# Kernel optimization log

Hardware: AMD Instinct MI355X
Metric: run time of the kernel (lower is better)

## Reference

```python
import jax, jax.numpy as jnp
import numpy as np

NEG_INF = -1e9  # matches tf mask value -1000000000.0
LEAKY_ALPHA = 0.2  # tf.nn.leaky_relu default


def setup_inputs() -> dict:
    key = jax.random.key(0)
    k1, k2, k3, k4 = jax.random.split(key, 4)
    B, N, F, U = 8, 2048, 128, 128
    X = jax.random.normal(k1, (B, N, F), dtype=jnp.float32)
    A = jax.random.randint(k2, (B, N, N), 0, 2, dtype=jnp.int32)
    W = jax.random.normal(k3, (F, U), dtype=jnp.float32) * 0.1
    a = jax.random.normal(k4, (2 * U, 1), dtype=jnp.float32) * 0.1
    return {"X": X, "A": A, "W": W, "a": a}


def reference(X, A, W, a):
    # H = X @ W : [B, N, U]
    H = jnp.einsum('bnf,fu->bnu', X, W)
    U = H.shape[-1]
    # Additive decomposition of the tile+concat: [H_i || H_j] @ a = H_i@a_src + H_j@a_dst
    a_src = a[:U, 0]   # [U]
    a_dst = a[U:, 0]   # [U]
    s = H @ a_src      # [B, N]
    t = H @ a_dst      # [B, N]
    e = s[:, :, None] + t[:, None, :]            # [B, N, N] pairwise logits
    e = jax.nn.leaky_relu(e, negative_slope=LEAKY_ALPHA)
    mask = jnp.where(A > 0, 0.0, NEG_INF).astype(e.dtype)
    attention = jax.nn.softmax(e + mask, axis=-1)  # [B, N, N]
    H_out = jnp.einsum('bij,bju->biu', attention, H)
    return jax.nn.relu(H_out)
```

## Files before the change

kernel.cpp:

```cpp
#include <hip/hip_runtime.h>
#include <hip/hip_bf16.h>


#define NEG_INF -1.0e9f

typedef __bf16 bf16x8 __attribute__((ext_vector_type(8)));
typedef unsigned short ushort8 __attribute__((ext_vector_type(8)));
typedef float f32x4 __attribute__((ext_vector_type(4)));

__device__ __forceinline__ unsigned short f2b(float x) {
    unsigned u = __builtin_bit_cast(unsigned, x);
    u += 0x7fffu + ((u >> 16) & 1u);
    return (unsigned short)(u >> 16);
}

__device__ __forceinline__ void gload_lds16(const void* g, void* l) {
    __builtin_amdgcn_global_load_lds(
        (const __attribute__((address_space(1))) void*)g,
        (__attribute__((address_space(3))) void*)l, 16, 0, 0);
}

__global__ __launch_bounds__(256) void k_h(const float* __restrict__ X,
                                           const float* __restrict__ W,
                                           const float* __restrict__ a,
                                           unsigned short* __restrict__ HT,
                                           float* __restrict__ sbuf,
                                           float* __restrict__ tbuf) {
    __shared__ unsigned short WT[128 * 136];

    const int tid  = threadIdx.x;
    const int w    = tid >> 6;
    const int lane = tid & 63;
    const int r    = lane & 15;
    const int cg   = lane >> 4;

    for (int i = tid; i < 16384; i += 256) {
        int u = i >> 7, f = i & 127;
        WT[u * 136 + f] = f2b(W[f * 128 + u]);
    }
    __syncthreads();

    const int row0 = blockIdx.x * 64 + w * 16;
    const int b    = row0 >> 11;
    const int n0   = row0 & 2047;
    const int arow = row0 + r;

    f32x4 acc[8] = {};

#pragma unroll
    for (int k0 = 0; k0 < 128; k0 += 32) {
        const float* xp = X + (size_t)arow * 128 + k0 + cg * 8;
        ushort8 xa;
#pragma unroll
        for (int j = 0; j < 8; j++) xa[j] = f2b(xp[j]);
        bf16x8 av = __builtin_bit_cast(bf16x8, xa);
#pragma unroll
        for (int ut = 0; ut < 8; ut++) {
            ushort8 wb = *(const ushort8*)(&WT[(ut * 16 + r) * 136 + k0 + cg * 8]);
            acc[ut] = __builtin_amdgcn_mfma_f32_16x16x32_bf16(
                av, __builtin_bit_cast(bf16x8, wb), acc[ut], 0, 0, 0);
        }
    }

    float sp[4] = {0.f, 0.f, 0.f, 0.f};
    float tp[4] = {0.f, 0.f, 0.f, 0.f};
#pragma unroll
    for (int ut = 0; ut < 8; ut++) {
        int u = ut * 16 + r;
        float as = a[u];
        float ad = a[128 + u];
#pragma unroll
        for (int reg = 0; reg < 4; reg++) {
            float h = acc[ut][reg];
            int nrow = n0 + cg * 4 + reg;
            HT[((size_t)b * 128 + u) * 2048 + nrow] = f2b(h);
            sp[reg] += h * as;
            tp[reg] += h * ad;
        }
    }
#pragma unroll
    for (int msk = 1; msk < 16; msk <<= 1) {
#pragma unroll
        for (int reg = 0; reg < 4; reg++) {
            sp[reg] += __shfl_xor(sp[reg], msk);
            tp[reg] += __shfl_xor(tp[reg], msk);
        }
    }
    if (r == 0) {
#pragma unroll
        for (int reg = 0; reg < 4; reg++) {
            int row = row0 + cg * 4 + reg;
            sbuf[row] = sp[reg];
            tbuf[row] = tp[reg];
        }
    }
}

__global__ __launch_bounds__(512, 4) void k_attn(const int* __restrict__ A,
                                                 const unsigned short* __restrict__ HT,
                                                 const float* __restrict__ sbuf,
                                                 const float* __restrict__ tbuf,
                                                 float* __restrict__ out) {
    __shared__ char smem[65536];
    __shared__ float dSm[4][2][16];

    const int tid  = threadIdx.x;
    const int w    = tid >> 6;
    const int lane = tid & 63;
    const int r    = lane & 15;
    const int cg   = lane >> 4;
    const int g    = w & 1;
    const int jq   = w >> 1;
    const int bid  = blockIdx.x;
    const int b    = bid & 7;
    const int it   = bid >> 3;
    const int i0   = it * 32;
    const int rot  = it & 15;

    const int irow = i0 + g * 16 + r;
    const float s_r = sbuf[b * 2048 + irow];
    const unsigned short* Hb = HT + ((size_t)b * 128) * 2048 + jq * 512;
    const int*   Aq = A    + ((size_t)(b * 2048 + irow)) * 2048 + jq * 512 + cg * 8;
    const float* Tq = tbuf + (size_t)b * 2048 + jq * 512 + cg * 8;

    const int srow = (lane >> 2);
    const int csrc = (lane & 3) ^ ((lane >> 2) & 3) ^ ((lane >> 4) & 3);
    char* const qbase = smem + jq * 16384;
    const unsigned short* src0 = Hb + (size_t)(g * 64 + srow) * 2048 + csrc * 8;
    const int rsl = ((r & 3) ^ ((r >> 2) & 3));

    f32x4 acc[8] = {};
    float den = 0.f;

    int4   aP[2][2];
    float4 tP[2][2];
    {
        const int j0 = rot * 32;
        const int j1 = ((1 + rot) & 15) * 32;
        aP[0][0] = *(const int4*)(Aq + j0);
        aP[0][1] = *(const int4*)(Aq + j0 + 4);
        tP[0][0] = *(const float4*)(Tq + j0);
        tP[0][1] = *(const float4*)(Tq + j0 + 4);
        aP[1][0] = *(const int4*)(Aq + j1);
        aP[1][1] = *(const int4*)(Aq + j1 + 4);
        tP[1][0] = *(const float4*)(Tq + j1);
        tP[1][1] = *(const float4*)(Tq + j1 + 4);
#pragma unroll
        for (int i = 0; i < 4; i++)
            gload_lds16(src0 + (size_t)i * 16 * 2048 + j0,
                        qbase + (g * 4 + i) * 1024);
    }
    __syncthreads();

#pragma unroll
    for (int k = 0; k < 16; ++k) {
        const int p = k & 1;

        int4   ca = aP[p][0],  cb = aP[p][1];
        float4 ct0 = tP[p][0], ct1 = tP[p][1];

        if (k < 15) {
            const int jn = ((k + 1 + rot) & 15) * 32;
            char* dst = qbase + (p ^ 1) * 8192;
#pragma unroll
            for (int i = 0; i < 4; i++)
                gload_lds16(src0 + (size_t)i * 16 * 2048 + jn,
                            dst + (g * 4 + i) * 1024);
        }
        if (k < 14) {
            const int ja = ((k + 2 + rot) & 15) * 32;
            aP[p][0] = *(const int4*)(Aq + ja);
            aP[p][1] = *(const int4*)(Aq + ja + 4);
            tP[p][0] = *(const float4*)(Tq + ja);
            tP[p][1] = *(const float4*)(Tq + ja + 4);
        }

        float tv[8] = {ct0.x, ct0.y, ct0.z, ct0.w, ct1.x, ct1.y, ct1.z, ct1.w};
        int   ai[8] = {ca.x, ca.y, ca.z, ca.w, cb.x, cb.y, cb.z, cb.w};
        bf16x8 pa;
#pragma unroll
        for (int jj = 0; jj < 8; jj++) {
            float x = s_r + tv[jj];
            float e = fmaxf(x, 0.2f * x);
            float pp = __expf(e - 16.0f);
            pp = ai[jj] > 0 ? pp : 0.f;
            den += pp;
            pa[jj] = (__bf16)pp;
        }

        if (k < 14)      asm volatile("s_waitcnt vmcnt(8)" ::: "memory");
        else if (k < 15) asm volatile("s_waitcnt vmcnt(4)" ::: "memory");
        else             asm volatile("s_waitcnt vmcnt(0)" ::: "memory");
        __builtin_amdgcn_s_barrier();
        __builtin_amdgcn_sched_barrier(0);

        const char* buf = qbase + p * 8192;
#pragma unroll
        for (int ut = 0; ut < 8; ut++) {
            ushort8 hb = *(const ushort8*)(buf + (ut * 16 + r) * 64 +
                                           ((cg ^ rsl) * 16));
            acc[ut] = __builtin_amdgcn_mfma_f32_16x16x32_bf16(
                pa, __builtin_bit_cast(bf16x8, hb), acc[ut], 0, 0, 0);
        }

        if (k < 15) {
            __builtin_amdgcn_s_barrier();
            __builtin_amdgcn_sched_barrier(0);
        }
    }

    den += __shfl_xor(den, 16);
    den += __shfl_xor(den, 32);

    __syncthreads();

    float* accS = (float*)smem;
    if (cg == 0) dSm[jq][g][r] = den;
    if (jq != 0) {
        const int rowIdx = ((jq - 1) * 2 + g) * 16 + cg * 4;
#pragma unroll
        for (int ut = 0; ut < 8; ut++)
#pragma unroll
            for (int reg = 0; reg < 4; reg++)
                accS[(rowIdx + reg) * 132 + ut * 16 + r] = acc[ut][reg];
    }
    __syncthreads();
    if (jq == 0) {
        float dinv[4];
#pragma unroll
        for (int reg = 0; reg < 4; reg++) {
            const int row = cg * 4 + reg;
            dinv[reg] = 1.0f / (dSm[0][g][row] + dSm[1][g][row] +
                                dSm[2][g][row] + dSm[3][g][row]);
        }
#pragma unroll
        for (int ut = 0; ut < 8; ut++) {
#pragma unroll
            for (int reg = 0; reg < 4; reg++) {
                const int lrow = cg * 4 + reg;
                float num = acc[ut][reg]
                          + accS[((0 * 2 + g) * 16 + lrow) * 132 + ut * 16 + r]
                          + accS[((1 * 2 + g) * 16 + lrow) * 132 + ut * 16 + r]
                          + accS[((2 * 2 + g) * 16 + lrow) * 132 + ut * 16 + r];
                float o = fmaxf(num * dinv[reg], 0.f);
                out[((size_t)(b * 2048 + i0 + g * 16 + lrow)) * 128 +
                    ut * 16 + r] = o;
            }
        }
    }
}

extern "C" void kernel_launch(void* const* d_in, const int* in_sizes, int n_in,
                              void* d_out, int out_size, void* d_ws, size_t ws_size,
                              hipStream_t stream) {
    const float* X = (const float*)d_in[0];
    const int*   A = (const int*)d_in[1];
    const float* W = (const float*)d_in[2];
    const float* a = (const float*)d_in[3];
    float* out = (float*)d_out;

    char* ws = (char*)d_ws;
    float*          sb  = (float*)(ws);
    float*          tb  = (float*)(ws + 65536);
    unsigned short* HT  = (unsigned short*)(ws + 131072);

    k_h<<<dim3(256), dim3(256), 0, stream>>>(X, W, a, HT, sb, tb);
    k_attn<<<dim3(512), dim3(512), 0, stream>>>(A, HT, sb, tb, out);
}
```

Measured before the change: 61.96 us.

## Process two 16-row groups per wave to reuse each H fragment across two MFMAs

The attention kernel drops from 8 waves to 4 waves per block. Each wave now handles both 16-row halves of the 32-row tile, so every H fragment read from LDS feeds two MFMAs and each wave stages the full 128-row H slice itself. This halves LDS reads of H per MFMA and cuts barrier participants, at the cost of doubled accumulator and prefetch registers per wave, fewer waves for latency hiding, and adjusted vmcnt thresholds.

```diff
diff --git a/kernel.cpp b/kernel.cpp
--- a/kernel.cpp
+++ b/kernel.cpp
@@ -96,59 +96,64 @@
     }
 }
 
-__global__ __launch_bounds__(512, 4) void k_attn(const int* __restrict__ A,
+__global__ __launch_bounds__(256, 2) void k_attn(const int* __restrict__ A,
                                                  const unsigned short* __restrict__ HT,
                                                  const float* __restrict__ sbuf,
                                                  const float* __restrict__ tbuf,
                                                  float* __restrict__ out) {
     __shared__ char smem[65536];
-    __shared__ float dSm[4][2][16];
+    __shared__ float dSm[4][32];
 
     const int tid  = threadIdx.x;
-    const int w    = tid >> 6;
+    const int jq   = tid >> 6;
     const int lane = tid & 63;
     const int r    = lane & 15;
     const int cg   = lane >> 4;
-    const int g    = w & 1;
-    const int jq   = w >> 1;
     const int bid  = blockIdx.x;
     const int b    = bid & 7;
     const int it   = bid >> 3;
     const int i0   = it * 32;
     const int rot  = it & 15;
 
-    const int irow = i0 + g * 16 + r;
-    const float s_r = sbuf[b * 2048 + irow];
+    const int irow0 = i0 + r;
+    const float s0 = sbuf[b * 2048 + irow0];
+    const float s1 = sbuf[b * 2048 + irow0 + 16];
     const unsigned short* Hb = HT + ((size_t)b * 128) * 2048 + jq * 512;
-    const int*   Aq = A    + ((size_t)(b * 2048 + irow)) * 2048 + jq * 512 + cg * 8;
-    const float* Tq = tbuf + (size_t)b * 2048 + jq * 512 + cg * 8;
+    const int*   Aq0 = A    + ((size_t)(b * 2048 + irow0)) * 2048 + jq * 512 + cg * 8;
+    const int*   Aq1 = Aq0 + 16 * 2048;
+    const float* Tq  = tbuf + (size_t)b * 2048 + jq * 512 + cg * 8;
 
     const int srow = (lane >> 2);
     const int csrc = (lane & 3) ^ ((lane >> 2) & 3) ^ ((lane >> 4) & 3);
     char* const qbase = smem + jq * 16384;
-    const unsigned short* src0 = Hb + (size_t)(g * 64 + srow) * 2048 + csrc * 8;
+    const unsigned short* src0 = Hb + (size_t)srow * 2048 + csrc * 8;
     const int rsl = ((r & 3) ^ ((r >> 2) & 3));
 
-    f32x4 acc[8] = {};
-    float den = 0.f;
-
-    int4   aP[2][2];
+    f32x4 acc0[8] = {};
+    f32x4 acc1[8] = {};
+    float den0 = 0.f, den1 = 0.f;
+
+    int4   aP0[2][2], aP1[2][2];
     float4 tP[2][2];
     {
         const int j0 = rot * 32;
         const int j1 = ((1 + rot) & 15) * 32;
-        aP[0][0] = *(const int4*)(Aq + j0);
-        aP[0][1] = *(const int4*)(Aq + j0 + 4);
-        tP[0][0] = *(const float4*)(Tq + j0);
-        tP[0][1] = *(const float4*)(Tq + j0 + 4);
-        aP[1][0] = *(const int4*)(Aq + j1);
-        aP[1][1] = *(const int4*)(Aq + j1 + 4);
-        tP[1][0] = *(const float4*)(Tq + j1);
-        tP[1][1] = *(const float4*)(Tq + j1 + 4);
-#pragma unroll
-        for (int i = 0; i < 4; i++)
+        aP0[0][0] = *(const int4*)(Aq0 + j0);
+        aP0[0][1] = *(const int4*)(Aq0 + j0 + 4);
+        aP1[0][0] = *(const int4*)(Aq1 + j0);
+        aP1[0][1] = *(const int4*)(Aq1 + j0 + 4);
+        tP[0][0]  = *(const float4*)(Tq + j0);
+        tP[0][1]  = *(const float4*)(Tq + j0 + 4);
+        aP0[1][0] = *(const int4*)(Aq0 + j1);
+        aP0[1][1] = *(const int4*)(Aq0 + j1 + 4);
+        aP1[1][0] = *(const int4*)(Aq1 + j1);
+        aP1[1][1] = *(const int4*)(Aq1 + j1 + 4);
+        tP[1][0]  = *(const float4*)(Tq + j1);
+        tP[1][1]  = *(const float4*)(Tq + j1 + 4);
+#pragma unroll
+        for (int i = 0; i < 8; i++)
             gload_lds16(src0 + (size_t)i * 16 * 2048 + j0,
-                        qbase + (g * 4 + i) * 1024);
+                        qbase + i * 1024);
     }
     __syncthreads();
 
@@ -156,40 +161,51 @@
     for (int k = 0; k < 16; ++k) {
         const int p = k & 1;
 
-        int4   ca = aP[p][0],  cb = aP[p][1];
-        float4 ct0 = tP[p][0], ct1 = tP[p][1];
+        int4   ca0 = aP0[p][0], ca1 = aP0[p][1];
+        int4   cb0 = aP1[p][0], cb1 = aP1[p][1];
+        float4 ct0 = tP[p][0],  ct1 = tP[p][1];
 
         if (k < 15) {
             const int jn = ((k + 1 + rot) & 15) * 32;
             char* dst = qbase + (p ^ 1) * 8192;
 #pragma unroll
-            for (int i = 0; i < 4; i++)
+            for (int i = 0; i < 8; i++)
                 gload_lds16(src0 + (size_t)i * 16 * 2048 + jn,
-                            dst + (g * 4 + i) * 1024);
+                            dst + i * 1024);
         }
         if (k < 14) {
             const int ja = ((k + 2 + rot) & 15) * 32;
-            aP[p][0] = *(const int4*)(Aq + ja);
-            aP[p][1] = *(const int4*)(Aq + ja + 4);
-            tP[p][0] = *(const float4*)(Tq + ja);
-            tP[p][1] = *(const float4*)(Tq + ja + 4);
+            aP0[p][0] = *(const int4*)(Aq0 + ja);
+            aP0[p][1] = *(const int4*)(Aq0 + ja + 4);
+            aP1[p][0] = *(const int4*)(Aq1 + ja);
+            aP1[p][1] = *(const int4*)(Aq1 + ja + 4);
+            tP[p][0]  = *(const float4*)(Tq + ja);
+            tP[p][1]  = *(const float4*)(Tq + ja + 4);
         }
 
         float tv[8] = {ct0.x, ct0.y, ct0.z, ct0.w, ct1.x, ct1.y, ct1.z, ct1.w};
-        int   ai[8] = {ca.x, ca.y, ca.z, ca.w, cb.x, cb.y, cb.z, cb.w};
-        bf16x8 pa;
+        int   a0i[8] = {ca0.x, ca0.y, ca0.z, ca0.w, ca1.x, ca1.y, ca1.z, ca1.w};
+        int   a1i[8] = {cb0.x, cb0.y, cb0.z, cb0.w, cb1.x, cb1.y, cb1.z, cb1.w};
+        bf16x8 pa0, pa1;
 #pragma unroll
         for (int jj = 0; jj < 8; jj++) {
-            float x = s_r + tv[jj];
-            float e = fmaxf(x, 0.2f * x);
-            float pp = __expf(e - 16.0f);
-            pp = ai[jj] > 0 ? pp : 0.f;
-            den += pp;
-            pa[jj] = (__bf16)pp;
-        }
-
-        if (k < 14)      asm volatile("s_waitcnt vmcnt(8)" ::: "memory");
-        else if (k < 15) asm volatile("s_waitcnt vmcnt(4)" ::: "memory");
+            float x0 = s0 + tv[jj];
+            float e0 = fmaxf(x0, 0.2f * x0);
+            float p0 = __expf(e0 - 16.0f);
+            p0 = a0i[jj] > 0 ? p0 : 0.f;
+            den0 += p0;
+            pa0[jj] = (__bf16)p0;
+
+            float x1 = s1 + tv[jj];
+            float e1 = fmaxf(x1, 0.2f * x1);
+            float p1 = __expf(e1 - 16.0f);
+            p1 = a1i[jj] > 0 ? p1 : 0.f;
+            den1 += p1;
+            pa1[jj] = (__bf16)p1;
+        }
+
+        if (k < 14)      asm volatile("s_waitcnt vmcnt(14)" ::: "memory");
+        else if (k < 15) asm volatile("s_waitcnt vmcnt(8)" ::: "memory");
         else             asm volatile("s_waitcnt vmcnt(0)" ::: "memory");
         __builtin_amdgcn_s_barrier();
         __builtin_amdgcn_sched_barrier(0);
@@ -199,8 +215,9 @@
         for (int ut = 0; ut < 8; ut++) {
             ushort8 hb = *(const ushort8*)(buf + (ut * 16 + r) * 64 +
                                            ((cg ^ rsl) * 16));
-            acc[ut] = __builtin_amdgcn_mfma_f32_16x16x32_bf16(
-                pa, __builtin_bit_cast(bf16x8, hb), acc[ut], 0, 0, 0);
+            bf16x8 hbv = __builtin_bit_cast(bf16x8, hb);
+            acc0[ut] = __builtin_amdgcn_mfma_f32_16x16x32_bf16(pa0, hbv, acc0[ut], 0, 0, 0);
+            acc1[ut] = __builtin_amdgcn_mfma_f32_16x16x32_bf16(pa1, hbv, acc1[ut], 0, 0, 0);
         }
 
         if (k < 15) {
@@ -209,42 +226,55 @@
         }
     }
 
-    den += __shfl_xor(den, 16);
-    den += __shfl_xor(den, 32);
+    den0 += __shfl_xor(den0, 16);
+    den0 += __shfl_xor(den0, 32);
+    den1 += __shfl_xor(den1, 16);
+    den1 += __shfl_xor(den1, 32);
 
     __syncthreads();
 
     float* accS = (float*)smem;
-    if (cg == 0) dSm[jq][g][r] = den;
+    if (cg == 0) { dSm[jq][r] = den0; dSm[jq][16 + r] = den1; }
     if (jq != 0) {
-        const int rowIdx = ((jq - 1) * 2 + g) * 16 + cg * 4;
+        const int base = (jq - 1) * 32;
 #pragma unroll
         for (int ut = 0; ut < 8; ut++)
 #pragma unroll
-            for (int reg = 0; reg < 4; reg++)
-                accS[(rowIdx + reg) * 132 + ut * 16 + r] = acc[ut][reg];
+            for (int reg = 0; reg < 4; reg++) {
+                accS[(base + cg * 4 + reg) * 132 + ut * 16 + r]      = acc0[ut][reg];
+                accS[(base + 16 + cg * 4 + reg) * 132 + ut * 16 + r] = acc1[ut][reg];
+            }
     }
     __syncthreads();
     if (jq == 0) {
-        float dinv[4];
-#pragma unroll
-        for (int reg = 0; reg < 4; reg++) {
-            const int row = cg * 4 + reg;
-            dinv[reg] = 1.0f / (dSm[0][g][row] + dSm[1][g][row] +
-                                dSm[2][g][row] + dSm[3][g][row]);
+        float dinv0[4], dinv1[4];
+#pragma unroll
+        for (int reg = 0; reg < 4; reg++) {
+            const int row0_ = cg * 4 + reg;
+            const int row1_ = 16 + cg * 4 + reg;
+            dinv0[reg] = 1.0f / (dSm[0][row0_] + dSm[1][row0_] +
+                                 dSm[2][row0_] + dSm[3][row0_]);
+            dinv1[reg] = 1.0f / (dSm[0][row1_] + dSm[1][row1_] +
+                                 dSm[2][row1_] + dSm[3][row1_]);
         }
 #pragma unroll
         for (int ut = 0; ut < 8; ut++) {
 #pragma unroll
             for (int reg = 0; reg < 4; reg++) {
-                const int lrow = cg * 4 + reg;
-                float num = acc[ut][reg]
-                          + accS[((0 * 2 + g) * 16 + lrow) * 132 + ut * 16 + r]
-                          + accS[((1 * 2 + g) * 16 + lrow) * 132 + ut * 16 + r]
-                          + accS[((2 * 2 + g) * 16 + lrow) * 132 + ut * 16 + r];
-                float o = fmaxf(num * dinv[reg], 0.f);
-                out[((size_t)(b * 2048 + i0 + g * 16 + lrow)) * 128 +
-                    ut * 16 + r] = o;
+                const int lr0 = cg * 4 + reg;
+                const int lr1 = 16 + cg * 4 + reg;
+                float n0 = acc0[ut][reg]
+                         + accS[(0 * 32 + lr0) * 132 + ut * 16 + r]
+                         + accS[(1 * 32 + lr0) * 132 + ut * 16 + r]
+                         + accS[(2 * 32 + lr0) * 132 + ut * 16 + r];
+                float n1 = acc1[ut][reg]
+                         + accS[(0 * 32 + lr1) * 132 + ut * 16 + r]
+                         + accS[(1 * 32 + lr1) * 132 + ut * 16 + r]
+                         + accS[(2 * 32 + lr1) * 132 + ut * 16 + r];
+                out[((size_t)(b * 2048 + i0 + lr0)) * 128 + ut * 16 + r] =
+                    fmaxf(n0 * dinv0[reg], 0.f);
+                out[((size_t)(b * 2048 + i0 + lr1)) * 128 + ut * 16 + r] =
+                    fmaxf(n1 * dinv1[reg], 0.f);
             }
         }
     }
@@ -265,5 +295,5 @@
     unsigned short* HT  = (unsigned short*)(ws + 131072);
 
     k_h<<<dim3(256), dim3(256), 0, stream>>>(X, W, a, HT, sb, tb);
-    k_attn<<<dim3(512), dim3(512), 0, stream>>>(A, HT, sb, tb, out);
-}
+    k_attn<<<dim3(512), dim3(256), 0, stream>>>(A, HT, sb, tb, out);
+}
```

Measured after the change: 60.01 us. -3.2%, faster.

## Load H fragments directly to registers, drop LDS staging and barriers

Applied to the files above, without the earlier changes.

The attention kernel stops staging H tiles in shared memory with global_load_lds and per-step barriers. Each wave now loads its MFMA B operands straight from global memory into registers and double-buffers them across the k loop. Blocks shrink to 256 threads covering 16 rows each, so twice as many blocks are launched. This removes LDS traffic and barrier stalls, but each H tile is fetched once per wave instead of once per block, roughly doubling global and L2 reads of H, and the loads are narrow per-lane accesses.

```diff
diff --git a/kernel.cpp b/kernel.cpp
--- a/kernel.cpp
+++ b/kernel.cpp
@@ -12,12 +12,6 @@
     unsigned u = __builtin_bit_cast(unsigned, x);
     u += 0x7fffu + ((u >> 16) & 1u);
     return (unsigned short)(u >> 16);
-}
-
-__device__ __forceinline__ void gload_lds16(const void* g, void* l) {
-    __builtin_amdgcn_global_load_lds(
-        (const __attribute__((address_space(1))) void*)g,
-        (__attribute__((address_space(3))) void*)l, 16, 0, 0);
 }
 
 __global__ __launch_bounds__(256) void k_h(const float* __restrict__ X,
@@ -96,47 +90,46 @@
     }
 }
 
-__global__ __launch_bounds__(512, 4) void k_attn(const int* __restrict__ A,
+__global__ __launch_bounds__(256, 4) void k_attn(const int* __restrict__ A,
                                                  const unsigned short* __restrict__ HT,
                                                  const float* __restrict__ sbuf,
                                                  const float* __restrict__ tbuf,
                                                  float* __restrict__ out) {
-    __shared__ char smem[65536];
-    __shared__ float dSm[4][2][16];
+    __shared__ float accS[3 * 16 * 132];
+    __shared__ float dSm[4][16];
 
     const int tid  = threadIdx.x;
-    const int w    = tid >> 6;
+    const int jq   = tid >> 6;
     const int lane = tid & 63;
     const int r    = lane & 15;
     const int cg   = lane >> 4;
-    const int g    = w & 1;
-    const int jq   = w >> 1;
     const int bid  = blockIdx.x;
     const int b    = bid & 7;
     const int it   = bid >> 3;
-    const int i0   = it * 32;
+    const int i0   = it * 16;
     const int rot  = it & 15;
 
-    const int irow = i0 + g * 16 + r;
+    const int irow = i0 + r;
     const float s_r = sbuf[b * 2048 + irow];
-    const unsigned short* Hb = HT + ((size_t)b * 128) * 2048 + jq * 512;
+    const unsigned short* Hrow = HT + ((size_t)b * 128 + r) * 2048 + jq * 512;
     const int*   Aq = A    + ((size_t)(b * 2048 + irow)) * 2048 + jq * 512 + cg * 8;
     const float* Tq = tbuf + (size_t)b * 2048 + jq * 512 + cg * 8;
 
-    const int srow = (lane >> 2);
-    const int csrc = (lane & 3) ^ ((lane >> 2) & 3) ^ ((lane >> 4) & 3);
-    char* const qbase = smem + jq * 16384;
-    const unsigned short* src0 = Hb + (size_t)(g * 64 + srow) * 2048 + csrc * 8;
-    const int rsl = ((r & 3) ^ ((r >> 2) & 3));
-
     f32x4 acc[8] = {};
     float den = 0.f;
 
+    ushort8 bA[4], bB[4];
     int4   aP[2][2];
     float4 tP[2][2];
+
     {
         const int j0 = rot * 32;
         const int j1 = ((1 + rot) & 15) * 32;
+#pragma unroll
+        for (int h = 0; h < 4; h++) {
+            bA[h] = *(const ushort8*)(Hrow + (size_t)(h * 16) * 2048 + j0 + cg * 8);
+            bB[h] = *(const ushort8*)(Hrow + (size_t)((h + 4) * 16) * 2048 + j0 + cg * 8);
+        }
         aP[0][0] = *(const int4*)(Aq + j0);
         aP[0][1] = *(const int4*)(Aq + j0 + 4);
         tP[0][0] = *(const float4*)(Tq + j0);
@@ -145,38 +138,17 @@
         aP[1][1] = *(const int4*)(Aq + j1 + 4);
         tP[1][0] = *(const float4*)(Tq + j1);
         tP[1][1] = *(const float4*)(Tq + j1 + 4);
-#pragma unroll
-        for (int i = 0; i < 4; i++)
-            gload_lds16(src0 + (size_t)i * 16 * 2048 + j0,
-                        qbase + (g * 4 + i) * 1024);
-    }
-    __syncthreads();
+    }
 
 #pragma unroll
     for (int k = 0; k < 16; ++k) {
         const int p = k & 1;
-
-        int4   ca = aP[p][0],  cb = aP[p][1];
-        float4 ct0 = tP[p][0], ct1 = tP[p][1];
-
-        if (k < 15) {
-            const int jn = ((k + 1 + rot) & 15) * 32;
-            char* dst = qbase + (p ^ 1) * 8192;
-#pragma unroll
-            for (int i = 0; i < 4; i++)
-                gload_lds16(src0 + (size_t)i * 16 * 2048 + jn,
-                            dst + (g * 4 + i) * 1024);
-        }
-        if (k < 14) {
-            const int ja = ((k + 2 + rot) & 15) * 32;
-            aP[p][0] = *(const int4*)(Aq + ja);
-            aP[p][1] = *(const int4*)(Aq + ja + 4);
-            tP[p][0] = *(const float4*)(Tq + ja);
-            tP[p][1] = *(const float4*)(Tq + ja + 4);
-        }
-
-        float tv[8] = {ct0.x, ct0.y, ct0.z, ct0.w, ct1.x, ct1.y, ct1.z, ct1.w};
-        int   ai[8] = {ca.x, ca.y, ca.z, ca.w, cb.x, cb.y, cb.z, cb.w};
+        const int jn = ((k + 1 + rot) & 15) * 32 + cg * 8;
+
+        float tv[8] = {tP[p][0].x, tP[p][0].y, tP[p][0].z, tP[p][0].w,
+                       tP[p][1].x, tP[p][1].y, tP[p][1].z, tP[p][1].w};
+        int   ai[8] = {aP[p][0].x, aP[p][0].y, aP[p][0].z, aP[p][0].w,
+                       aP[p][1].x, aP[p][1].y, aP[p][1].z, aP[p][1].w};
         bf16x8 pa;
 #pragma unroll
         for (int jj = 0; jj < 8; jj++) {
@@ -188,41 +160,51 @@
             pa[jj] = (__bf16)pp;
         }
 
-        if (k < 14)      asm volatile("s_waitcnt vmcnt(8)" ::: "memory");
-        else if (k < 15) asm volatile("s_waitcnt vmcnt(4)" ::: "memory");
-        else             asm volatile("s_waitcnt vmcnt(0)" ::: "memory");
-        __builtin_amdgcn_s_barrier();
+#pragma unroll
+        for (int h = 0; h < 4; h++) {
+            acc[h] = __builtin_amdgcn_mfma_f32_16x16x32_bf16(
+                pa, __builtin_bit_cast(bf16x8, bA[h]), acc[h], 0, 0, 0);
+        }
+        if (k < 15) {
+#pragma unroll
+            for (int h = 0; h < 4; h++)
+                bA[h] = *(const ushort8*)(Hrow + (size_t)(h * 16) * 2048 + jn);
+        }
         __builtin_amdgcn_sched_barrier(0);
 
-        const char* buf = qbase + p * 8192;
-#pragma unroll
-        for (int ut = 0; ut < 8; ut++) {
-            ushort8 hb = *(const ushort8*)(buf + (ut * 16 + r) * 64 +
-                                           ((cg ^ rsl) * 16));
-            acc[ut] = __builtin_amdgcn_mfma_f32_16x16x32_bf16(
-                pa, __builtin_bit_cast(bf16x8, hb), acc[ut], 0, 0, 0);
-        }
-
+#pragma unroll
+        for (int h = 0; h < 4; h++) {
+            acc[h + 4] = __builtin_amdgcn_mfma_f32_16x16x32_bf16(
+                pa, __builtin_bit_cast(bf16x8, bB[h]), acc[h + 4], 0, 0, 0);
+        }
         if (k < 15) {
-            __builtin_amdgcn_s_barrier();
-            __builtin_amdgcn_sched_barrier(0);
-        }
+#pragma unroll
+            for (int h = 0; h < 4; h++)
+                bB[h] = *(const ushort8*)(Hrow + (size_t)((h + 4) * 16) * 2048 + jn);
+        }
+        __builtin_amdgcn_sched_barrier(0);
+
+        if (k < 14) {
+            const int ja = ((k + 2 + rot) & 15) * 32;
+            aP[p][0] = *(const int4*)(Aq + ja);
+            aP[p][1] = *(const int4*)(Aq + ja + 4);
+            tP[p][0] = *(const float4*)(Tq + ja);
+            tP[p][1] = *(const float4*)(Tq + ja + 4);
+        }
+        __builtin_amdgcn_sched_barrier(0);
     }
 
     den += __shfl_xor(den, 16);
     den += __shfl_xor(den, 32);
 
-    __syncthreads();
-
-    float* accS = (float*)smem;
-    if (cg == 0) dSm[jq][g][r] = den;
+    if (cg == 0) dSm[jq][r] = den;
     if (jq != 0) {
-        const int rowIdx = ((jq - 1) * 2 + g) * 16 + cg * 4;
+        const int base = (jq - 1) * 16;
 #pragma unroll
         for (int ut = 0; ut < 8; ut++)
 #pragma unroll
             for (int reg = 0; reg < 4; reg++)
-                accS[(rowIdx + reg) * 132 + ut * 16 + r] = acc[ut][reg];
+                accS[(base + cg * 4 + reg) * 132 + ut * 16 + r] = acc[ut][reg];
     }
     __syncthreads();
     if (jq == 0) {
@@ -230,21 +212,20 @@
 #pragma unroll
         for (int reg = 0; reg < 4; reg++) {
             const int row = cg * 4 + reg;
-            dinv[reg] = 1.0f / (dSm[0][g][row] + dSm[1][g][row] +
-                                dSm[2][g][row] + dSm[3][g][row]);
+            dinv[reg] = 1.0f / (dSm[0][row] + dSm[1][row] +
+                                dSm[2][row] + dSm[3][row]);
         }
 #pragma unroll
         for (int ut = 0; ut < 8; ut++) {
 #pragma unroll
             for (int reg = 0; reg < 4; reg++) {
-                const int lrow = cg * 4 + reg;
+                const int lr = cg * 4 + reg;
                 float num = acc[ut][reg]
-                          + accS[((0 * 2 + g) * 16 + lrow) * 132 + ut * 16 + r]
-                          + accS[((1 * 2 + g) * 16 + lrow) * 132 + ut * 16 + r]
-                          + accS[((2 * 2 + g) * 16 + lrow) * 132 + ut * 16 + r];
-                float o = fmaxf(num * dinv[reg], 0.f);
-                out[((size_t)(b * 2048 + i0 + g * 16 + lrow)) * 128 +
-                    ut * 16 + r] = o;
+                          + accS[(0 * 16 + lr) * 132 + ut * 16 + r]
+                          + accS[(1 * 16 + lr) * 132 + ut * 16 + r]
+                          + accS[(2 * 16 + lr) * 132 + ut * 16 + r];
+                out[((size_t)(b * 2048 + i0 + lr)) * 128 + ut * 16 + r] =
+                    fmaxf(num * dinv[reg], 0.f);
             }
         }
     }
@@ -265,5 +246,5 @@
     unsigned short* HT  = (unsigned short*)(ws + 131072);
 
     k_h<<<dim3(256), dim3(256), 0, stream>>>(X, W, a, HT, sb, tb);
-    k_attn<<<dim3(512), dim3(512), 0, stream>>>(A, HT, sb, tb, out);
-}
+    k_attn<<<dim3(1024), dim3(256), 0, stream>>>(A, HT, sb, tb, out);
+}
```

After: 94.56 us. 1.53x slower.
